# Optimization experiments

Measured on AMD Instinct MI355X. Metric: run time of the kernel, lower is better.

The kernel has to match this reference:

```python
import jax, jax.numpy as jnp
import numpy as np

ALPHA = 0.2        # LeakyReLU slope
N_NODES = 50000
N_REL = 500


def l2norm(x):
    n = jnp.linalg.norm(x, axis=1, keepdims=True)
    return x / jnp.maximum(n, 1e-12)


def gat_layer(x, edge, eemb, a, a2, concat):
    # x: [N, F]; edge: [2, E] (edge[0]=target, edge[1]=source); eemb: [E, R]
    dst = edge[0]
    h = jnp.concatenate([x[dst], x[edge[1]], eemb], axis=1)          # [E, 2F+R]
    m = h @ a.T                                                       # [E, out]
    p = -jax.nn.leaky_relu(m @ a2[0], ALPHA)                          # [E]
    e = jnp.exp(p)
    rowsum = jax.ops.segment_sum(e, dst, num_segments=N_NODES)       # [N]
    rowsum = jnp.where(rowsum == 0.0, 1e-12, rowsum)
    hp = jax.ops.segment_sum(e[:, None] * m, dst, num_segments=N_NODES) / rowsum[:, None]
    return jax.nn.elu(hp) if concat else hp


def setup_inputs() -> dict:
    key = jax.random.key(0)
    ks = jax.random.split(key, 12)
    E, ENH = 150000, 30000
    D, NHID, H = 200, 100, 2
    return {
        "entity_embeddings": jax.random.normal(ks[0], (N_NODES, D), jnp.float32),
        "relation_embeddings": jax.random.normal(ks[1], (N_REL, D), jnp.float32),
        "W_entities": jax.random.normal(ks[2], (D, NHID * H), jnp.float32) * 0.1,
        "W_gat": jax.random.normal(ks[3], (D, NHID * H), jnp.float32) * 0.1,
        "a_heads": jax.random.normal(ks[4], (H, NHID, 2 * D + D), jnp.float32) * 0.1,
        "a2_heads": jax.random.normal(ks[5], (H, 1, NHID), jnp.float32) * 0.1,
        "a_out": jax.random.normal(ks[6], (NHID * H, 3 * NHID * H), jnp.float32) * 0.1,
        "a2_out": jax.random.normal(ks[7], (1, NHID * H), jnp.float32) * 0.1,
        "batch_entities": jax.random.randint(ks[8], (20000,), 0, N_NODES),
        "edge_list": jax.random.randint(ks[9], (2, E), 0, N_NODES),
        "edge_type": jax.random.randint(ks[10], (E,), 0, N_REL),
        "train_indices_nhop": jax.random.randint(ks[11], (ENH, 4), 0, N_REL),
    }


def reference(entity_embeddings, relation_embeddings, W_entities, W_gat,
              a_heads, a2_heads, a_out, a2_out,
              batch_entities, edge_list, edge_type, train_indices_nhop):
    x = l2norm(entity_embeddings)
    # n-hop edges: (target, source) = (col 3, col 0); relation pair = (col 1, col 2)
    edge_nhop = jnp.stack([train_indices_nhop[:, 3], train_indices_nhop[:, 0]])
    edge_all = jnp.concatenate([edge_list, edge_nhop], axis=1)       # [2, E+Enh]
    eemb1 = jnp.concatenate([
        relation_embeddings[edge_type],
        relation_embeddings[train_indices_nhop[:, 1]] + relation_embeddings[train_indices_nhop[:, 2]],
    ], axis=0)
    # multi-head sparse attention (concat=True -> elu inside)
    heads = jax.vmap(lambda a, a2: gat_layer(x, edge_all, eemb1, a, a2, True))(a_heads, a2_heads)
    x1 = jnp.transpose(heads, (1, 0, 2)).reshape(x.shape[0], -1)     # [N, H*nhid]
    out_rel = relation_embeddings @ W_gat                             # [R, H*nhid]
    eemb2 = jnp.concatenate([
        out_rel[edge_type],
        out_rel[train_indices_nhop[:, 1]] + out_rel[train_indices_nhop[:, 2]],
    ], axis=0)
    out_ent = jax.nn.elu(gat_layer(x1, edge_all, eemb2, a_out, a2_out, False))
    mask = jnp.zeros((x.shape[0],), x.dtype).at[batch_entities].set(1.0)
    out_ent = l2norm(x @ W_entities + mask[:, None] * out_ent)
    return out_ent, out_rel, mask
```

## Files before the change

### kernel.cpp

```cpp
#include <hip/hip_runtime.h>
#include <hip/hip_bf16.h>
#include <math.h>

#define DD   200
#define NHID 100
#define OD   200
#define KP   224
#define PBS  448
#define LDSW 40

typedef __attribute__((ext_vector_type(8))) short short8;
typedef __attribute__((ext_vector_type(4))) float f32x4;

static inline int cdiv(int a, int b) { return (a + b - 1) / b; }

__device__ inline float toF(float x) { return x; }
__device__ inline float toF(__hip_bfloat16 x) { return __bfloat162float(x); }
__device__ inline void storeC(float v, float* p) { *p = v; }
__device__ inline void storeC(float v, __hip_bfloat16* p) { *p = __float2bfloat16(v); }
__device__ inline short bf16s(float f) {
    __hip_bfloat16 h = __float2bfloat16(f);
    short s; __builtin_memcpy(&s, &h, 2); return s;
}
__device__ inline float bfLo(unsigned u) { return __uint_as_float(u << 16); }
__device__ inline float bfHi(unsigned u) { return __uint_as_float(u & 0xFFFF0000u); }
__device__ inline float readlaneF(float v, int l) {
    return __uint_as_float((unsigned)__builtin_amdgcn_readlane((int)__float_as_uint(v), l));
}

__global__ __launch_bounds__(256)
void rownorm_inv_k(const float* __restrict__ in, float* __restrict__ sc, int M, int Dd)
{
    int wave = (blockIdx.x * blockDim.x + threadIdx.x) >> 6;
    int lane = threadIdx.x & 63;
    if (wave >= M) return;
    float ss = 0.f;
    for (int k = lane; k < Dd; k += 64) {
        float x = in[(size_t)wave * Dd + k];
        ss += x * x;
    }
    for (int o = 32; o > 0; o >>= 1) ss += __shfl_down(ss, o);
    if (lane == 0) sc[wave] = 1.f / fmaxf(sqrtf(ss), 1e-12f);
}

__global__ void prep_bt_l1(const float* __restrict__ ah, __hip_bfloat16* __restrict__ Bt)
{
    int c = blockIdx.x, k = threadIdx.x;
    if (k >= KP) return;
    int seg = c / 100, idx = c - seg * 100;
    int h = seg & 1, off = (seg >> 1) * 200;
    float v = (k < 200) ? ah[(size_t)(h * 100 + idx) * 600 + off + k] : 0.f;
    Bt[(size_t)c * KP + k] = __float2bfloat16(v);
}
__global__ void prep_bt_l2(const float* __restrict__ ao, __hip_bfloat16* __restrict__ Bt)
{
    int c = blockIdx.x, k = threadIdx.x;
    if (k >= KP) return;
    int row = (c < 200) ? c : c - 200;
    int off = (c < 200) ? 0 : 200;
    float v = (k < 200) ? ao[(size_t)row * 600 + off + k] : 0.f;
    Bt[(size_t)c * KP + k] = __float2bfloat16(v);
}
__global__ void prep_bt_fin(const float* __restrict__ W, __hip_bfloat16* __restrict__ Bt)
{
    int c = blockIdx.x, k = threadIdx.x;
    if (k >= KP) return;
    float v = (c < 200 && k < 200) ? W[(size_t)k * 200 + c] : 0.f;
    Bt[(size_t)c * KP + k] = __float2bfloat16(v);
}

__global__ __launch_bounds__(512)
void l1_both_k(const float* __restrict__ ent, const float* __restrict__ nscale,
               const __hip_bfloat16* __restrict__ Bt,
               const float* __restrict__ a2h,
               __hip_bfloat16* __restrict__ x1,
               __hip_bfloat16* __restrict__ pB,
               float* __restrict__ s1,
               int M)
{
    __shared__ __align__(16) __hip_bfloat16 Bs[400 * LDSW];
    int tid = threadIdx.x, wave = tid >> 6, lane = tid & 63;
    int quad = lane >> 4, l16 = lane & 15;
    int m0 = blockIdx.x * 128;
    int arow = m0 + wave * 16 + l16;
    bool rok = arow < M;
    float nsc = rok ? nscale[arow] : 0.f;
    const float* arp = ent + (size_t)arow * DD;
    int orow = m0 + wave * 16 + quad * 4;

    if (blockIdx.y == 0) {
        f32x4 acc[25];
#pragma unroll
        for (int t = 0; t < 25; t++) acc[t] = (f32x4){0.f, 0.f, 0.f, 0.f};

        short8 stg[4];
#pragma unroll
        for (int i = 0; i < 4; i++) {
            int idx = tid + i * 512;
            if (idx < 1600) {
                int r = idx >> 2, c8 = idx & 3;
                stg[i] = *(const short8*)(Bt + (size_t)r * KP + c8 * 8);
            }
        }
        for (int ch = 0; ch < 7; ch++) {
            int kb = ch * 32 + quad * 8;
            float av[8];
            if (rok && kb + 8 <= DD) {
                const float4* p = (const float4*)(arp + kb);
                float4 u0 = p[0], u1 = p[1];
                av[0] = u0.x; av[1] = u0.y; av[2] = u0.z; av[3] = u0.w;
                av[4] = u1.x; av[5] = u1.y; av[6] = u1.z; av[7] = u1.w;
            } else {
#pragma unroll
                for (int j = 0; j < 8; j++) av[j] = (rok && kb + j < DD) ? arp[kb + j] : 0.f;
            }
#pragma unroll
            for (int i = 0; i < 4; i++) {
                int idx = tid + i * 512;
                if (idx < 1600) {
                    int r = idx >> 2, c8 = idx & 3;
                    *(short8*)(Bs + r * LDSW + c8 * 8) = stg[i];
                }
            }
            __syncthreads();
            if (ch < 6) {
                int kb2 = (ch + 1) * 32;
#pragma unroll
                for (int i = 0; i < 4; i++) {
                    int idx = tid + i * 512;
                    if (idx < 1600) {
                        int r = idx >> 2, c8 = idx & 3;
                        stg[i] = *(const short8*)(Bt + (size_t)r * KP + kb2 + c8 * 8);
                    }
                }
            }
            short8 a;
#pragma unroll
            for (int j = 0; j < 8; j++) a[j] = bf16s(av[j] * nsc);
            const __hip_bfloat16* bp = Bs + (size_t)l16 * LDSW + quad * 8;
#pragma unroll
            for (int t = 0; t < 25; t++) {
                short8 b = *(const short8*)(bp + (size_t)t * 16 * LDSW);
                acc[t] = __builtin_amdgcn_mfma_f32_16x16x32_bf16(a, b, acc[t], 0, 0, 0);
            }
            __syncthreads();
        }

        float d0[4] = {0,0,0,0}, d1[4] = {0,0,0,0}, d2[4] = {0,0,0,0}, d3[4] = {0,0,0,0};
#pragma unroll
        for (int t = 0; t < 25; t++) {
            int c = t * 16 + l16;
            int seg = c / 100, idx = c - seg * 100;
            float w = a2h[(seg & 1) * 100 + idx];
#pragma unroll
            for (int i = 0; i < 4; i++) {
                float v = acc[t][i];
                float vw = v * w;
                if (seg == 0) d0[i] += vw;
                else if (seg == 1) d1[i] += vw;
                else if (seg == 2) d2[i] += vw;
                else d3[i] += vw;
                int gm = orow + i;
                if (gm < M) {
                    if (seg < 2) x1[(size_t)gm * KP + c] = __float2bfloat16(v);
                    else pB[(size_t)gm * PBS + idx * 2 + (seg - 2)] = __float2bfloat16(v);
                }
            }
        }
        if (l16 < 12)
#pragma unroll
            for (int i = 0; i < 4; i++) {
                int gm = orow + i;
                if (gm < M) *(unsigned*)(x1 + (size_t)gm * KP + 200 + 2 * l16) = 0u;
            }
#pragma unroll
        for (int msk = 1; msk < 16; msk <<= 1)
#pragma unroll
            for (int i = 0; i < 4; i++) {
                d0[i] += __shfl_xor(d0[i], msk);
                d1[i] += __shfl_xor(d1[i], msk);
                d2[i] += __shfl_xor(d2[i], msk);
                d3[i] += __shfl_xor(d3[i], msk);
            }
        if (l16 == 0)
#pragma unroll
            for (int i = 0; i < 4; i++) {
                int gm = orow + i;
                if (gm < M) {
                    s1[gm] = d0[i]; s1[M + gm] = d1[i];
                    float2 sv; sv.x = d2[i]; sv.y = d3[i];
                    *(float2*)((char*)pB + (size_t)gm * (PBS * 2) + 400) = sv;
                }
            }
    } else {
        f32x4 acc2[13];
#pragma unroll
        for (int t = 0; t < 13; t++) acc2[t] = (f32x4){0.f, 0.f, 0.f, 0.f};

        short8 stg2[2];
#pragma unroll
        for (int i = 0; i < 2; i++) {
            int idx = tid + i * 512;
            if (idx < 832) {
                int r = idx >> 2, c8 = idx & 3;
                stg2[i] = *(const short8*)(Bt + (size_t)(400 + r) * KP + c8 * 8);
            }
        }
        for (int ch = 0; ch < 7; ch++) {
            int kb = ch * 32 + quad * 8;
            float av[8];
            if (rok && kb + 8 <= DD) {
                const float4* p = (const float4*)(arp + kb);
                float4 u0 = p[0], u1 = p[1];
                av[0] = u0.x; av[1] = u0.y; av[2] = u0.z; av[3] = u0.w;
                av[4] = u1.x; av[5] = u1.y; av[6] = u1.z; av[7] = u1.w;
            } else {
#pragma unroll
                for (int j = 0; j < 8; j++) av[j] = (rok && kb + j < DD) ? arp[kb + j] : 0.f;
            }
#pragma unroll
            for (int i = 0; i < 2; i++) {
                int idx = tid + i * 512;
                if (idx < 832) {
                    int r = idx >> 2, c8 = idx & 3;
                    *(short8*)(Bs + r * LDSW + c8 * 8) = stg2[i];
                }
            }
            __syncthreads();
            if (ch < 6) {
                int kb2 = (ch + 1) * 32;
#pragma unroll
                for (int i = 0; i < 2; i++) {
                    int idx = tid + i * 512;
                    if (idx < 832) {
                        int r = idx >> 2, c8 = idx & 3;
                        stg2[i] = *(const short8*)(Bt + (size_t)(400 + r) * KP + kb2 + c8 * 8);
                    }
                }
            }
            short8 a;
#pragma unroll
            for (int j = 0; j < 8; j++) a[j] = bf16s(av[j] * nsc);
            const __hip_bfloat16* bp = Bs + (size_t)l16 * LDSW + quad * 8;
#pragma unroll
            for (int t = 0; t < 13; t++) {
                short8 b = *(const short8*)(bp + (size_t)t * 16 * LDSW);
                acc2[t] = __builtin_amdgcn_mfma_f32_16x16x32_bf16(a, b, acc2[t], 0, 0, 0);
            }
            __syncthreads();
        }
#pragma unroll
        for (int t = 0; t < 13; t++) {
            int c2 = t * 16 + l16;
#pragma unroll
            for (int i = 0; i < 4; i++) {
                int gm = orow + i;
                if (c2 < OD && gm < M)
                    pB[(size_t)gm * PBS + 224 + c2] = __float2bfloat16(acc2[t][i]);
            }
        }
    }
}

__global__ __launch_bounds__(512)
void l2_proj_k(const __hip_bfloat16* __restrict__ x1,
               const __hip_bfloat16* __restrict__ Bt,
               const float* __restrict__ a2o,
               float* __restrict__ x1A1,
               __hip_bfloat16* __restrict__ x1A2,
               float* __restrict__ s1, int M)
{
    __shared__ __align__(16) __hip_bfloat16 Bs[400 * LDSW];
    int tid = threadIdx.x, wave = tid >> 6, lane = tid & 63;
    int quad = lane >> 4, l16 = lane & 15;
    int m0 = blockIdx.x * 128;
    int arow = m0 + wave * 16 + l16;
    bool rok = arow < M;
    const __hip_bfloat16* arp = x1 + (size_t)arow * KP;

    f32x4 acc[25];
#pragma unroll
    for (int t = 0; t < 25; t++) acc[t] = (f32x4){0.f, 0.f, 0.f, 0.f};

    short8 stg[4];
#pragma unroll
    for (int i = 0; i < 4; i++) {
        int idx = tid + i * 512;
        if (idx < 1600) {
            int r = idx >> 2, c8 = idx & 3;
            stg[i] = *(const short8*)(Bt + (size_t)r * KP + c8 * 8);
        }
    }

    for (int ch = 0; ch < 7; ch++) {
        short8 a = (short8){0,0,0,0,0,0,0,0};
        if (rok) a = *(const short8*)(arp + ch * 32 + quad * 8);
#pragma unroll
        for (int i = 0; i < 4; i++) {
            int idx = tid + i * 512;
            if (idx < 1600) {
                int r = idx >> 2, c8 = idx & 3;
                *(short8*)(Bs + r * LDSW + c8 * 8) = stg[i];
            }
        }
        __syncthreads();
        if (ch < 6) {
            int kb2 = (ch + 1) * 32;
#pragma unroll
            for (int i = 0; i < 4; i++) {
                int idx = tid + i * 512;
                if (idx < 1600) {
                    int r = idx >> 2, c8 = idx & 3;
                    stg[i] = *(const short8*)(Bt + (size_t)r * KP + kb2 + c8 * 8);
                }
            }
        }
        const __hip_bfloat16* bp = Bs + (size_t)l16 * LDSW + quad * 8;
#pragma unroll
        for (int t = 0; t < 25; t++) {
            short8 b = *(const short8*)(bp + (size_t)t * 16 * LDSW);
            acc[t] = __builtin_amdgcn_mfma_f32_16x16x32_bf16(a, b, acc[t], 0, 0, 0);
        }
        __syncthreads();
    }

    int orow = m0 + wave * 16 + quad * 4;
    float dA[4] = {0,0,0,0}, dB[4] = {0,0,0,0};
#pragma unroll
    for (int t = 0; t < 25; t++) {
        int c = t * 16 + l16;
        bool first = c < 200;
        int cc = first ? c : c - 200;
        float w = a2o[cc];
#pragma unroll
        for (int i = 0; i < 4; i++) {
            float v = acc[t][i];
            int gm = orow + i;
            if (first) {
                dA[i] += v * w;
                if (gm < M) x1A1[(size_t)gm * OD + c] = v;
            } else {
                dB[i] += v * w;
                if (gm < M) x1A2[(size_t)gm * PBS + cc] = __float2bfloat16(v);
            }
        }
    }
#pragma unroll
    for (int msk = 1; msk < 16; msk <<= 1)
#pragma unroll
        for (int i = 0; i < 4; i++) {
            dA[i] += __shfl_xor(dA[i], msk);
            dB[i] += __shfl_xor(dB[i], msk);
        }
    if (l16 == 0)
#pragma unroll
        for (int i = 0; i < 4; i++) {
            int gm = orow + i;
            if (gm < M) {
                s1[gm] = dA[i];
                *(float*)((char*)x1A2 + (size_t)gm * (PBS * 2) + 400) = dB[i];
            }
        }
}

#define KPAD 48
template<bool BTr, typename AT, typename CT>
__global__ __launch_bounds__(256)
void gemm_mfma_k(const AT* __restrict__ A, int lda, const float* __restrict__ ascale,
                 const float* __restrict__ B, int ldb, int colOff,
                 CT* __restrict__ C, int ldc, int cs, int co,
                 int M, int Nc, int K)
{
    __shared__ __align__(16) __hip_bfloat16 As[64][KPAD];
    __shared__ __align__(16) __hip_bfloat16 Bs[64][KPAD];
    int tid  = threadIdx.x;
    int wave = tid >> 6, lane = tid & 63;
    int quad = lane >> 4, l16 = lane & 15;
    int n0 = blockIdx.x * 64, m0 = blockIdx.y * 64;
    f32x4 acc[4];
#pragma unroll
    for (int t = 0; t < 4; t++) acc[t] = (f32x4){0.f, 0.f, 0.f, 0.f};

    for (int k0 = 0; k0 < K; k0 += 32) {
        {
            int m = tid >> 2, kc = (tid & 3) * 8;
            int gm = m0 + m;
            float scale = (ascale && gm < M) ? ascale[gm] : 1.f;
#pragma unroll
            for (int j = 0; j < 8; j++) {
                int gk = k0 + kc + j;
                float v = 0.f;
                if (gm < M && gk < K) v = toF(A[(size_t)gm * lda + gk]) * scale;
                As[m][kc + j] = __float2bfloat16(v);
            }
        }
        if (BTr) {
            int n = tid >> 2, kc = (tid & 3) * 8;
            int gn = n0 + n;
#pragma unroll
            for (int j = 0; j < 8; j++) {
                int gk = k0 + kc + j;
                float v = 0.f;
                if (gn < Nc && gk < K) v = B[(size_t)gn * ldb + colOff + gk];
                Bs[n][kc + j] = __float2bfloat16(v);
            }
        } else {
            int n = tid & 63, kq = tid >> 6;
            int gn = n0 + n;
#pragma unroll
            for (int j = 0; j < 8; j++) {
                int gk = k0 + kq * 8 + j;
                float v = 0.f;
                if (gn < Nc && gk < K) v = B[(size_t)gk * ldb + gn];
                Bs[n][kq * 8 + j] = __float2bfloat16(v);
            }
        }
        __syncthreads();
        short8 a = *(const short8*)&As[wave * 16 + l16][quad * 8];
#pragma unroll
        for (int t = 0; t < 4; t++) {
            short8 b = *(const short8*)&Bs[t * 16 + l16][quad * 8];
            acc[t] = __builtin_amdgcn_mfma_f32_16x16x32_bf16(a, b, acc[t], 0, 0, 0);
        }
        __syncthreads();
    }
#pragma unroll
    for (int t = 0; t < 4; t++) {
        int gn = n0 + t * 16 + l16;
        if (gn >= Nc) continue;
#pragma unroll
        for (int i = 0; i < 4; i++) {
            int gm = m0 + wave * 16 + quad * 4 + i;
            if (gm < M) storeC(acc[t][i], &C[(size_t)gm * ldc + (size_t)gn * cs + co]);
        }
    }
}

template<typename T>
__global__ __launch_bounds__(256)
void rowdot_k(const T* __restrict__ mat, int ld, int coff, int ks,
              const float* __restrict__ vec,
              float* __restrict__ outp, int os, int oo, int M, int Dd)
{
    int wave = (blockIdx.x * blockDim.x + threadIdx.x) >> 6;
    int lane = threadIdx.x & 63;
    if (wave >= M) return;
    float s = 0.f;
    for (int k = lane; k < Dd; k += 64)
        s += toF(mat[(size_t)wave * ld + coff + (size_t)k * ks]) * vec[k];
    for (int o = 32; o > 0; o >>= 1) s += __shfl_down(s, o);
    if (lane == 0) outp[wave * os + oo] = s;
}

__device__ inline void decode_edge(const int* __restrict__ el, int E,
                                   const int* __restrict__ etype,
                                   const int* __restrict__ tin, int e,
                                   int& dst, int& src, int& r1, int& r2)
{
    if (e < E) { dst = el[e]; src = el[E + e]; r1 = etype[e]; r2 = -1; }
    else {
        int j = e - E;
        dst = tin[j * 4 + 3]; src = tin[j * 4 + 0];
        r1 = tin[j * 4 + 1];  r2 = tin[j * 4 + 2];
    }
}

__global__ void hist_k(const int* __restrict__ el, int E, const int* __restrict__ etype,
                       const int* __restrict__ tin, int Etot, int* __restrict__ cnt)
{
    int e = blockIdx.x * blockDim.x + threadIdx.x;
    if (e >= Etot) return;
    int dst, src, r1, r2; decode_edge(el, E, etype, tin, e, dst, src, r1, r2);
    atomicAdd(&cnt[dst], 1);
}

__global__ __launch_bounds__(1024)
void scan1_k(const int* __restrict__ cnt, int* __restrict__ start,
             int* __restrict__ aux, int n)
{
    __shared__ int tmp[1024];
    int i = blockIdx.x * 1024 + threadIdx.x;
    int v = (i < n) ? cnt[i] : 0;
    tmp[threadIdx.x] = v;
    __syncthreads();
    for (int o = 1; o < 1024; o <<= 1) {
        int t = (threadIdx.x >= (unsigned)o) ? tmp[threadIdx.x - o] : 0;
        __syncthreads();
        tmp[threadIdx.x] += t;
        __syncthreads();
    }
    if (i < n) start[i] = tmp[threadIdx.x] - v;
    if (threadIdx.x == 1023) aux[blockIdx.x] = tmp[1023];
}

__global__ void scan2_k(int* __restrict__ aux, int nb)
{
    if (threadIdx.x == 0 && blockIdx.x == 0) {
        int s = 0;
        for (int i = 0; i < nb; i++) { int v = aux[i]; aux[i] = s; s += v; }
    }
}

__global__ __launch_bounds__(1024)
void scan3_k(int* __restrict__ start, const int* __restrict__ aux, int n, int Etot)
{
    int i = blockIdx.x * 1024 + threadIdx.x;
    if (i < n) start[i] += aux[blockIdx.x];
    if (i == 0) start[n] = Etot;
}

__global__ void fill_k(const int* __restrict__ el, int E, const int* __restrict__ etype,
                       const int* __restrict__ tin, int Etot,
                       const int* __restrict__ start, int* __restrict__ fill,
                       int2* __restrict__ csr)
{
    int e = blockIdx.x * blockDim.x + threadIdx.x;
    if (e >= Etot) return;
    int dst, src, r1, r2; decode_edge(el, E, etype, tin, e, dst, src, r1, r2);
    int p = start[dst] + atomicAdd(&fill[dst], 1);
    unsigned r2s = (r2 >= 0) ? (unsigned)r2 : 0xFFFFu;
    csr[p] = make_int2(src, (int)((r2s << 16) | (unsigned)r1));
}

__global__ __launch_bounds__(256)
void gather_l1_k(const int* __restrict__ start, const int2* __restrict__ csr,
                 const float* __restrict__ s1,
                 const float* __restrict__ srel2,
                 const __hip_bfloat16* __restrict__ pB,
                 const float* __restrict__ rpf2,
                 __hip_bfloat16* __restrict__ x1, int N)
{
    int n = (blockIdx.x * blockDim.x + threadIdx.x) >> 6;
    int lane = threadIdx.x & 63;
    if (n >= N) return;
    int b0 = __builtin_amdgcn_readfirstlane(start[n]);
    int b1 = __builtin_amdgcn_readfirstlane(start[n + 1]);
    float s1h0 = s1[n], s1h1 = s1[N + n];
    float rsl0 = 0.f, rsl1 = 0.f;
    float2 acc0 = {0.f, 0.f};
    float2 acc1 = {0.f, 0.f};
    int k0 = lane;
    bool k1ok = lane < 36;
    int k1c = k1ok ? (lane + 64) : 0;

    for (int c0 = b0; c0 < b1; c0 += 64) {
        int cnt = min(64, b1 - c0);
        float w0 = 0.f, w1 = 0.f;
        int srcL = 0, eyL = 0;
        if (lane < cnt) {
            int2 eg = csr[c0 + lane];
            srcL = eg.x; eyL = eg.y;
            int r1 = eyL & 0xFFFF;
            unsigned r2u = (unsigned)eyL >> 16;
            float2 sA = *(const float2*)((const char*)pB + (size_t)(unsigned)srcL * (PBS * 2) + 400);
            float2 sr = *(const float2*)(srel2 + r1 * 2);
            float z0 = s1h0 + sA.x + sr.x;
            float z1 = s1h1 + sA.y + sr.y;
            if (r2u != 0xFFFFu) {
                float2 sr2v = *(const float2*)(srel2 + r2u * 2);
                z0 += sr2v.x; z1 += sr2v.y;
            }
            w0 = expf(-(z0 > 0.f ? z0 : 0.2f * z0));
            w1 = expf(-(z1 > 0.f ? z1 : 0.2f * z1));
            rsl0 += w0; rsl1 += w1;
        }
        for (int e0 = 0; e0 < cnt; e0 += 4) {
            int ec = min(4, cnt - e0);
            unsigned pw0[4], pw1[4];
#pragma unroll
            for (int u = 0; u < 4; u++) {
                if (u < ec) {
                    int s = __builtin_amdgcn_readlane(srcL, e0 + u);
                    const __hip_bfloat16* rA = pB + (size_t)(unsigned)s * PBS;
                    pw0[u] = *(const unsigned*)(rA + 2 * k0);
                    pw1[u] = *(const unsigned*)(rA + 2 * k1c);
                }
            }
#pragma unroll
            for (int u = 0; u < 4; u++) {
                if (u < ec) {
                    int ey = __builtin_amdgcn_readlane(eyL, e0 + u);
                    int r1 = ey & 0xFFFF;
                    unsigned r2u = (unsigned)ey >> 16;
                    float we0 = readlaneF(w0, e0 + u);
                    float we1 = readlaneF(w1, e0 + u);
                    const float2* q1 = (const float2*)(rpf2 + (unsigned)r1 * 200);
                    float2 q1a = q1[k0], q1b = q1[k1c];
                    float v00 = bfLo(pw0[u]) + q1a.x;
                    float v01 = bfHi(pw0[u]) + q1a.y;
                    float v10 = bfLo(pw1[u]) + q1b.x;
                    float v11 = bfHi(pw1[u]) + q1b.y;
                    if (r2u != 0xFFFFu) {
                        const float2* q2 = (const float2*)(rpf2 + r2u * 200);
                        float2 q2a = q2[k0], q2b = q2[k1c];
                        v00 += q2a.x; v01 += q2a.y;
                        v10 += q2b.x; v11 += q2b.y;
                    }
                    acc0.x += we0 * v00; acc0.y += we1 * v01;
                    acc1.x += we0 * v10; acc1.y += we1 * v11;
                }
            }
        }
    }

#pragma unroll
    for (int o = 1; o < 64; o <<= 1) {
        rsl0 += __shfl_xor(rsl0, o);
        rsl1 += __shfl_xor(rsl1, o);
    }
    float i0 = rsl0 > 0.f ? 1.f / rsl0 : 0.f;
    float i1 = rsl1 > 0.f ? 1.f / rsl1 : 0.f;
    __hip_bfloat16* xr = x1 + (size_t)n * KP;
    float hp;
    hp = rsl0 > 0.f ? toF(xr[k0]) + acc0.x * i0 : 0.f;
    xr[k0] = __float2bfloat16(hp > 0.f ? hp : expf(hp) - 1.f);
    hp = rsl1 > 0.f ? toF(xr[100 + k0]) + acc0.y * i1 : 0.f;
    xr[100 + k0] = __float2bfloat16(hp > 0.f ? hp : expf(hp) - 1.f);
    if (k1ok) {
        int k1 = lane + 64;
        hp = rsl0 > 0.f ? toF(xr[k1]) + acc1.x * i0 : 0.f;
        xr[k1] = __float2bfloat16(hp > 0.f ? hp : expf(hp) - 1.f);
        hp = rsl1 > 0.f ? toF(xr[100 + k1]) + acc1.y * i1 : 0.f;
        xr[100 + k1] = __float2bfloat16(hp > 0.f ? hp : expf(hp) - 1.f);
    }
}

__global__ __launch_bounds__(256)
void gather_l2_k(const int* __restrict__ start, const int2* __restrict__ csr,
                 const float* __restrict__ s1,
                 const float* __restrict__ srel,
                 const __hip_bfloat16* __restrict__ x1A2,
                 const float* __restrict__ rpf,
                 const float* __restrict__ maskf,
                 float* __restrict__ outent, int N)
{
    int n = (blockIdx.x * blockDim.x + threadIdx.x) >> 6;
    int lane = threadIdx.x & 63;
    if (n >= N) return;
    int b0 = __builtin_amdgcn_readfirstlane(start[n]);
    int b1 = __builtin_amdgcn_readfirstlane(start[n + 1]);
    float s1n = s1[n];
    float rsl = 0.f;
    float2 a0 = {0.f, 0.f};
    float2 a1 = {0.f, 0.f};
    int j0 = 2 * lane;
    bool j1ok = lane < 36;
    int j1 = j1ok ? (128 + 2 * lane) : 0;

    for (int c0 = b0; c0 < b1; c0 += 64) {
        int cnt = min(64, b1 - c0);
        float w = 0.f;
        int srcL = 0, eyL = 0;
        if (lane < cnt) {
            int2 eg = csr[c0 + lane];
            srcL = eg.x; eyL = eg.y;
            int r1 = eyL & 0xFFFF;
            unsigned r2u = (unsigned)eyL >> 16;
            float s2v = *(const float*)((const char*)x1A2 + (size_t)(unsigned)srcL * (PBS * 2) + 400);
            float sr = srel[r1];
            if (r2u != 0xFFFFu) sr += srel[r2u];
            float z = s1n + s2v + sr;
            w = expf(-(z > 0.f ? z : 0.2f * z));
            rsl += w;
        }
        for (int e0 = 0; e0 < cnt; e0 += 4) {
            int ec = min(4, cnt - e0);
            unsigned xw0[4], xw1[4];
#pragma unroll
            for (int u = 0; u < 4; u++) {
                if (u < ec) {
                    int s = __builtin_amdgcn_readlane(srcL, e0 + u);
                    const __hip_bfloat16* xs = x1A2 + (size_t)(unsigned)s * PBS;
                    xw0[u] = *(const unsigned*)(xs + j0);
                    xw1[u] = *(const unsigned*)(xs + j1);
                }
            }
#pragma unroll
            for (int u = 0; u < 4; u++) {
                if (u < ec) {
                    int ey = __builtin_amdgcn_readlane(eyL, e0 + u);
                    int r1 = ey & 0xFFFF;
                    unsigned r2u = (unsigned)ey >> 16;
                    float we = readlaneF(w, e0 + u);
                    const float* q1 = rpf + (unsigned)r1 * 200;
                    float2 q1a = *(const float2*)(q1 + j0);
                    float2 q1b = *(const float2*)(q1 + j1);
                    float v0x = bfLo(xw0[u]) + q1a.x;
                    float v0y = bfHi(xw0[u]) + q1a.y;
                    float v1x = bfLo(xw1[u]) + q1b.x;
                    float v1y = bfHi(xw1[u]) + q1b.y;
                    if (r2u != 0xFFFFu) {
                        const float* q2 = rpf + r2u * 200;
                        float2 q2a = *(const float2*)(q2 + j0);
                        float2 q2b = *(const float2*)(q2 + j1);
                        v0x += q2a.x; v0y += q2a.y;
                        v1x += q2b.x; v1y += q2b.y;
                    }
                    a0.x += we * v0x; a0.y += we * v0y;
                    a1.x += we * v1x; a1.y += we * v1y;
                }
            }
        }
    }

#pragma unroll
    for (int o = 1; o < 64; o <<= 1) rsl += __shfl_xor(rsl, o);
    float inv = rsl > 0.f ? 1.f / rsl : 0.f;
    float mk = maskf[n];
    float* orow = outent + (size_t)n * 200;
    const __hip_bfloat16* ew = x1A2 + (size_t)n * PBS + 224;

    float2 o0 = *(const float2*)(orow + j0);
    unsigned e0b = *(const unsigned*)(ew + j0);
    float h0x = rsl > 0.f ? o0.x + a0.x * inv : 0.f;
    float h0y = rsl > 0.f ? o0.y + a0.y * inv : 0.f;
    float v0x = mk * (h0x > 0.f ? h0x : expf(h0x) - 1.f) + bfLo(e0b);
    float v0y = mk * (h0y > 0.f ? h0y : expf(h0y) - 1.f) + bfHi(e0b);
    float ssq = v0x * v0x + v0y * v0y;
    float v1x = 0.f, v1y = 0.f;
    if (j1ok) {
        float2 o1 = *(const float2*)(orow + j1);
        unsigned e1b = *(const unsigned*)(ew + j1);
        float h1x = rsl > 0.f ? o1.x + a1.x * inv : 0.f;
        float h1y = rsl > 0.f ? o1.y + a1.y * inv : 0.f;
        v1x = mk * (h1x > 0.f ? h1x : expf(h1x) - 1.f) + bfLo(e1b);
        v1y = mk * (h1y > 0.f ? h1y : expf(h1y) - 1.f) + bfHi(e1b);
        ssq += v1x * v1x + v1y * v1y;
    }
#pragma unroll
    for (int o = 1; o < 64; o <<= 1) ssq += __shfl_xor(ssq, o);
    float sc = 1.f / fmaxf(sqrtf(ssq), 1e-12f);
    float2 r0; r0.x = v0x * sc; r0.y = v0y * sc;
    *(float2*)(orow + j0) = r0;
    if (j1ok) {
        float2 r1; r1.x = v1x * sc; r1.y = v1y * sc;
        *(float2*)(orow + j1) = r1;
    }
}

__global__ void scatter_mask_k(const int* __restrict__ batch, int NB,
                               float* __restrict__ masko)
{
    int i = blockIdx.x * blockDim.x + threadIdx.x;
    if (i >= NB) return;
    masko[batch[i]] = 1.0f;
}

extern "C" void kernel_launch(void* const* d_in, const int* in_sizes, int n_in,
                              void* d_out, int out_size, void* d_ws, size_t ws_size,
                              hipStream_t stream)
{
    const float* ent      = (const float*)d_in[0];
    const float* rel      = (const float*)d_in[1];
    const float* W_ent    = (const float*)d_in[2];
    const float* W_gat    = (const float*)d_in[3];
    const float* a_heads  = (const float*)d_in[4];
    const float* a2_heads = (const float*)d_in[5];
    const float* a_out    = (const float*)d_in[6];
    const float* a2_out   = (const float*)d_in[7];
    const int* batch = (const int*)d_in[8];
    const int* el    = (const int*)d_in[9];
    const int* etype = (const int*)d_in[10];
    const int* tin   = (const int*)d_in[11];

    const int N   = in_sizes[0] / DD;
    const int R   = in_sizes[1] / DD;
    const int NB  = in_sizes[8];
    const int E   = in_sizes[9] / 2;
    const int ENH = in_sizes[11] / 4;
    const int Etot = E + ENH;

    char* ws = (char*)d_ws;
    size_t off = 0;
    auto take = [&](size_t bytes) { size_t o = off; off += (bytes + 255) & ~(size_t)255; return o; };
    size_t o_R1   = take((size_t)N * KP * 2);
    size_t o_R2   = take((size_t)N * PBS * 2);
    size_t o_rpf  = take((size_t)2 * R * 100 * 4);
    size_t o_bt1  = take((size_t)400 * KP * 2);
    size_t o_btf  = take((size_t)208 * KP * 2);
    size_t o_bt2  = take((size_t)400 * KP * 2);
    size_t o_nsc  = take((size_t)N * 4);
    size_t o_s1   = take((size_t)2 * N * 4);
    size_t o_srel = take((size_t)2 * R * 4);
    size_t o_csr  = take((size_t)Etot * 8);
    size_t o_str  = take((size_t)(N + 1) * 4);
    size_t o_aux  = take((size_t)64 * 4);

    __hip_bfloat16* x1   = (__hip_bfloat16*)(ws + o_R1);
    __hip_bfloat16* pB   = (__hip_bfloat16*)(ws + o_R2);
    __hip_bfloat16* x1A2 = (__hip_bfloat16*)(ws + o_R2);
    float* rpf2   = (float*)(ws + o_rpf);
    __hip_bfloat16* bt1 = (__hip_bfloat16*)(ws + o_bt1);
    __hip_bfloat16* btf = (__hip_bfloat16*)(ws + o_btf);
    __hip_bfloat16* bt2 = (__hip_bfloat16*)(ws + o_bt2);
    float* nscale = (float*)(ws + o_nsc);
    float* s1     = (float*)(ws + o_s1);
    float* srel2  = (float*)(ws + o_srel);
    int2*  csr    = (int2*)(ws + o_csr);
    int*   cnt    = (int*)(ws + o_s1);
    int*   startA = (int*)(ws + o_str);
    int*   aux    = (int*)(ws + o_aux);

    float* out       = (float*)d_out;
    float* out_ent   = out;
    float* out_rel_o = out + (size_t)N * OD;
    float* out_mask  = out + (size_t)N * OD + (size_t)R * OD;

    const int nblk2 = cdiv(N, 128);
    const int nbScan = cdiv(N, 1024);

    rownorm_inv_k<<<cdiv(N, 4), 256, 0, stream>>>(ent, nscale, N, DD);
    prep_bt_l1<<<400, 256, 0, stream>>>(a_heads, bt1);
    prep_bt_fin<<<208, 256, 0, stream>>>(W_ent, btf);
    prep_bt_l2<<<400, 256, 0, stream>>>(a_out, bt2);
    gemm_mfma_k<false, float, float><<<dim3(cdiv(OD, 64), cdiv(R, 64)), 256, 0, stream>>>(
        rel, DD, nullptr, W_gat, OD, 0, out_rel_o, OD, 1, 0, R, OD, DD);

    hipMemsetAsync(cnt, 0, (size_t)N * 4, stream);
    hist_k<<<cdiv(Etot, 256), 256, 0, stream>>>(el, E, etype, tin, Etot, cnt);
    scan1_k<<<nbScan, 1024, 0, stream>>>(cnt, startA, aux, N);
    scan2_k<<<1, 64, 0, stream>>>(aux, nbScan);
    scan3_k<<<nbScan, 1024, 0, stream>>>(startA, aux, N, Etot);
    hipMemsetAsync(cnt, 0, (size_t)N * 4, stream);
    fill_k<<<cdiv(Etot, 256), 256, 0, stream>>>(el, E, etype, tin, Etot, startA, cnt, csr);

    l1_both_k<<<dim3(nblk2, 2), 512, 0, stream>>>(ent, nscale, bt1, a2_heads, x1, pB, s1, N);
    for (int h = 0; h < 2; h++) {
        const float* ah  = a_heads + (size_t)h * NHID * 600;
        const float* a2h = a2_heads + (size_t)h * NHID;
        gemm_mfma_k<true, float, float><<<dim3(cdiv(NHID, 64), cdiv(R, 64)), 256, 0, stream>>>(
            rel, DD, nullptr, ah, 600, 400, rpf2, 200, 2, h, R, NHID, DD);
        rowdot_k<float><<<cdiv(R, 4), 256, 0, stream>>>(
            rpf2, 200, h, 2, a2h, srel2, 2, h, R, NHID);
    }
    gather_l1_k<<<cdiv(N, 4), 256, 0, stream>>>(
        startA, csr, s1, srel2, pB, rpf2, x1, N);

    l2_proj_k<<<nblk2, 512, 0, stream>>>(x1, bt2, a2_out, out_ent, x1A2, s1, N);
    gemm_mfma_k<true, float, float><<<dim3(cdiv(OD, 64), cdiv(R, 64)), 256, 0, stream>>>(
        out_rel_o, OD, nullptr, a_out, 600, 400, rpf2, OD, 1, 0, R, OD, OD);
    rowdot_k<float><<<cdiv(R, 4), 256, 0, stream>>>(rpf2, OD, 0, 1, a2_out, srel2, 1, 0, R, OD);

    hipMemsetAsync(out_mask, 0, (size_t)N * 4, stream);
    scatter_mask_k<<<cdiv(NB, 256), 256, 0, stream>>>(batch, NB, out_mask);
    gather_l2_k<<<cdiv(N, 4), 256, 0, stream>>>(
        startA, csr, s1, srel2, x1A2, rpf2, out_mask, out_ent, N);
}
```

Baseline: 450.7 us.

## Split projection GEMMs into uniform 208-column blocks across more grid slices

The layer-1 and layer-2 projection kernels now split the output columns into equal 208-wide slices selected by blockIdx.y (3 slices for layer 1, 2 for layer 2), replacing the uneven 400+200 split and the single 400-column block. Each block holds 13 accumulator tiles instead of 25 and uses a smaller LDS buffer, which should raise occupancy and balance the work across blocks. The weight-transpose prep kernels are re-laid out with padded 208-row groups to match. The cost is that every slice re-reads the A rows (entity embeddings or x1) and repeats the normalisation and conversion work.

```diff
diff --git a/kernel.cpp b/kernel.cpp
--- a/kernel.cpp
+++ b/kernel.cpp
@@ -47,18 +47,23 @@
 {
     int c = blockIdx.x, k = threadIdx.x;
     if (k >= KP) return;
-    int seg = c / 100, idx = c - seg * 100;
-    int h = seg & 1, off = (seg >> 1) * 200;
-    float v = (k < 200) ? ah[(size_t)(h * 100 + idx) * 600 + off + k] : 0.f;
+    int g = (c >= 208) ? 1 : 0;
+    int cc = c - g * 208;
+    float v = 0.f;
+    if (cc < 200 && k < 200) {
+        int hh = (cc >= 100) ? 1 : 0;
+        int idx = cc - hh * 100;
+        v = ah[(size_t)(hh * 100 + idx) * 600 + g * 200 + k];
+    }
     Bt[(size_t)c * KP + k] = __float2bfloat16(v);
 }
 __global__ void prep_bt_l2(const float* __restrict__ ao, __hip_bfloat16* __restrict__ Bt)
 {
     int c = blockIdx.x, k = threadIdx.x;
     if (k >= KP) return;
-    int row = (c < 200) ? c : c - 200;
-    int off = (c < 200) ? 0 : 200;
-    float v = (k < 200) ? ao[(size_t)row * 600 + off + k] : 0.f;
+    int g = (c >= 208) ? 1 : 0;
+    int cc = c - g * 208;
+    float v = (cc < 200 && k < 200) ? ao[(size_t)cc * 600 + g * 200 + k] : 0.f;
     Bt[(size_t)c * KP + k] = __float2bfloat16(v);
 }
 __global__ void prep_bt_fin(const float* __restrict__ W, __hip_bfloat16* __restrict__ Bt)
@@ -78,188 +83,139 @@
                float* __restrict__ s1,
                int M)
 {
-    __shared__ __align__(16) __hip_bfloat16 Bs[400 * LDSW];
+    __shared__ __align__(16) __hip_bfloat16 Bs[208 * LDSW];
     int tid = threadIdx.x, wave = tid >> 6, lane = tid & 63;
     int quad = lane >> 4, l16 = lane & 15;
+    int f = blockIdx.y;
+    int rowbase = f * 208;
     int m0 = blockIdx.x * 128;
     int arow = m0 + wave * 16 + l16;
     bool rok = arow < M;
     float nsc = rok ? nscale[arow] : 0.f;
     const float* arp = ent + (size_t)arow * DD;
     int orow = m0 + wave * 16 + quad * 4;
-
-    if (blockIdx.y == 0) {
-        f32x4 acc[25];
-#pragma unroll
-        for (int t = 0; t < 25; t++) acc[t] = (f32x4){0.f, 0.f, 0.f, 0.f};
-
-        short8 stg[4];
-#pragma unroll
-        for (int i = 0; i < 4; i++) {
-            int idx = tid + i * 512;
-            if (idx < 1600) {
-                int r = idx >> 2, c8 = idx & 3;
-                stg[i] = *(const short8*)(Bt + (size_t)r * KP + c8 * 8);
-            }
-        }
-        for (int ch = 0; ch < 7; ch++) {
-            int kb = ch * 32 + quad * 8;
-            float av[8];
-            if (rok && kb + 8 <= DD) {
-                const float4* p = (const float4*)(arp + kb);
-                float4 u0 = p[0], u1 = p[1];
-                av[0] = u0.x; av[1] = u0.y; av[2] = u0.z; av[3] = u0.w;
-                av[4] = u1.x; av[5] = u1.y; av[6] = u1.z; av[7] = u1.w;
-            } else {
-#pragma unroll
-                for (int j = 0; j < 8; j++) av[j] = (rok && kb + j < DD) ? arp[kb + j] : 0.f;
-            }
-#pragma unroll
-            for (int i = 0; i < 4; i++) {
-                int idx = tid + i * 512;
-                if (idx < 1600) {
-                    int r = idx >> 2, c8 = idx & 3;
-                    *(short8*)(Bs + r * LDSW + c8 * 8) = stg[i];
-                }
-            }
-            __syncthreads();
-            if (ch < 6) {
-                int kb2 = (ch + 1) * 32;
-#pragma unroll
-                for (int i = 0; i < 4; i++) {
-                    int idx = tid + i * 512;
-                    if (idx < 1600) {
-                        int r = idx >> 2, c8 = idx & 3;
-                        stg[i] = *(const short8*)(Bt + (size_t)r * KP + kb2 + c8 * 8);
-                    }
-                }
-            }
-            short8 a;
-#pragma unroll
-            for (int j = 0; j < 8; j++) a[j] = bf16s(av[j] * nsc);
-            const __hip_bfloat16* bp = Bs + (size_t)l16 * LDSW + quad * 8;
-#pragma unroll
-            for (int t = 0; t < 25; t++) {
-                short8 b = *(const short8*)(bp + (size_t)t * 16 * LDSW);
-                acc[t] = __builtin_amdgcn_mfma_f32_16x16x32_bf16(a, b, acc[t], 0, 0, 0);
-            }
-            __syncthreads();
-        }
-
-        float d0[4] = {0,0,0,0}, d1[4] = {0,0,0,0}, d2[4] = {0,0,0,0}, d3[4] = {0,0,0,0};
-#pragma unroll
-        for (int t = 0; t < 25; t++) {
-            int c = t * 16 + l16;
-            int seg = c / 100, idx = c - seg * 100;
-            float w = a2h[(seg & 1) * 100 + idx];
-#pragma unroll
-            for (int i = 0; i < 4; i++) {
-                float v = acc[t][i];
-                float vw = v * w;
-                if (seg == 0) d0[i] += vw;
-                else if (seg == 1) d1[i] += vw;
-                else if (seg == 2) d2[i] += vw;
-                else d3[i] += vw;
-                int gm = orow + i;
-                if (gm < M) {
-                    if (seg < 2) x1[(size_t)gm * KP + c] = __float2bfloat16(v);
-                    else pB[(size_t)gm * PBS + idx * 2 + (seg - 2)] = __float2bfloat16(v);
-                }
-            }
-        }
-        if (l16 < 12)
-#pragma unroll
-            for (int i = 0; i < 4; i++) {
-                int gm = orow + i;
-                if (gm < M) *(unsigned*)(x1 + (size_t)gm * KP + 200 + 2 * l16) = 0u;
-            }
-#pragma unroll
-        for (int msk = 1; msk < 16; msk <<= 1)
-#pragma unroll
-            for (int i = 0; i < 4; i++) {
-                d0[i] += __shfl_xor(d0[i], msk);
-                d1[i] += __shfl_xor(d1[i], msk);
-                d2[i] += __shfl_xor(d2[i], msk);
-                d3[i] += __shfl_xor(d3[i], msk);
-            }
-        if (l16 == 0)
-#pragma unroll
-            for (int i = 0; i < 4; i++) {
-                int gm = orow + i;
-                if (gm < M) {
-                    s1[gm] = d0[i]; s1[M + gm] = d1[i];
-                    float2 sv; sv.x = d2[i]; sv.y = d3[i];
-                    *(float2*)((char*)pB + (size_t)gm * (PBS * 2) + 400) = sv;
-                }
-            }
-    } else {
-        f32x4 acc2[13];
-#pragma unroll
-        for (int t = 0; t < 13; t++) acc2[t] = (f32x4){0.f, 0.f, 0.f, 0.f};
-
-        short8 stg2[2];
+    const __hip_bfloat16* Bsrc = Bt + (size_t)rowbase * KP;
+
+    f32x4 acc[13];
+#pragma unroll
+    for (int t = 0; t < 13; t++) acc[t] = (f32x4){0.f, 0.f, 0.f, 0.f};
+
+    short8 stg[2];
+#pragma unroll
+    for (int i = 0; i < 2; i++) {
+        int idx = tid + i * 512;
+        if (idx < 832) {
+            int r = idx >> 2, c8 = idx & 3;
+            stg[i] = *(const short8*)(Bsrc + (size_t)r * KP + c8 * 8);
+        }
+    }
+    for (int ch = 0; ch < 7; ch++) {
+        int kb = ch * 32 + quad * 8;
+        float av[8];
+        if (rok && kb + 8 <= DD) {
+            const float4* p = (const float4*)(arp + kb);
+            float4 u0 = p[0], u1 = p[1];
+            av[0] = u0.x; av[1] = u0.y; av[2] = u0.z; av[3] = u0.w;
+            av[4] = u1.x; av[5] = u1.y; av[6] = u1.z; av[7] = u1.w;
+        } else {
+#pragma unroll
+            for (int j = 0; j < 8; j++) av[j] = (rok && kb + j < DD) ? arp[kb + j] : 0.f;
+        }
 #pragma unroll
         for (int i = 0; i < 2; i++) {
             int idx = tid + i * 512;
             if (idx < 832) {
                 int r = idx >> 2, c8 = idx & 3;
-                stg2[i] = *(const short8*)(Bt + (size_t)(400 + r) * KP + c8 * 8);
-            }
-        }
-        for (int ch = 0; ch < 7; ch++) {
-            int kb = ch * 32 + quad * 8;
-            float av[8];
-            if (rok && kb + 8 <= DD) {
-                const float4* p = (const float4*)(arp + kb);
-                float4 u0 = p[0], u1 = p[1];
-                av[0] = u0.x; av[1] = u0.y; av[2] = u0.z; av[3] = u0.w;
-                av[4] = u1.x; av[5] = u1.y; av[6] = u1.z; av[7] = u1.w;
-            } else {
-#pragma unroll
-                for (int j = 0; j < 8; j++) av[j] = (rok && kb + j < DD) ? arp[kb + j] : 0.f;
-            }
+                *(short8*)(Bs + r * LDSW + c8 * 8) = stg[i];
+            }
+        }
+        __syncthreads();
+        if (ch < 6) {
+            int kb2 = (ch + 1) * 32;
 #pragma unroll
             for (int i = 0; i < 2; i++) {
                 int idx = tid + i * 512;
                 if (idx < 832) {
                     int r = idx >> 2, c8 = idx & 3;
-                    *(short8*)(Bs + r * LDSW + c8 * 8) = stg2[i];
+                    stg[i] = *(const short8*)(Bsrc + (size_t)r * KP + kb2 + c8 * 8);
                 }
             }
-            __syncthreads();
-            if (ch < 6) {
-                int kb2 = (ch + 1) * 32;
-#pragma unroll
-                for (int i = 0; i < 2; i++) {
-                    int idx = tid + i * 512;
-                    if (idx < 832) {
-                        int r = idx >> 2, c8 = idx & 3;
-                        stg2[i] = *(const short8*)(Bt + (size_t)(400 + r) * KP + kb2 + c8 * 8);
-                    }
-                }
-            }
-            short8 a;
-#pragma unroll
-            for (int j = 0; j < 8; j++) a[j] = bf16s(av[j] * nsc);
-            const __hip_bfloat16* bp = Bs + (size_t)l16 * LDSW + quad * 8;
-#pragma unroll
-            for (int t = 0; t < 13; t++) {
-                short8 b = *(const short8*)(bp + (size_t)t * 16 * LDSW);
-                acc2[t] = __builtin_amdgcn_mfma_f32_16x16x32_bf16(a, b, acc2[t], 0, 0, 0);
-            }
-            __syncthreads();
-        }
+        }
+        short8 a;
+#pragma unroll
+        for (int j = 0; j < 8; j++) a[j] = bf16s(av[j] * nsc);
+        const __hip_bfloat16* bp = Bs + (size_t)l16 * LDSW + quad * 8;
 #pragma unroll
         for (int t = 0; t < 13; t++) {
-            int c2 = t * 16 + l16;
+            short8 b = *(const short8*)(bp + (size_t)t * 16 * LDSW);
+            acc[t] = __builtin_amdgcn_mfma_f32_16x16x32_bf16(a, b, acc[t], 0, 0, 0);
+        }
+        __syncthreads();
+    }
+
+    if (f == 2) {
+#pragma unroll
+        for (int t = 0; t < 13; t++) {
+            int cc = t * 16 + l16;
 #pragma unroll
             for (int i = 0; i < 4; i++) {
                 int gm = orow + i;
-                if (c2 < OD && gm < M)
-                    pB[(size_t)gm * PBS + 224 + c2] = __float2bfloat16(acc2[t][i]);
-            }
-        }
-    }
+                if (cc < OD && gm < M)
+                    pB[(size_t)gm * PBS + 224 + cc] = __float2bfloat16(acc[t][i]);
+            }
+        }
+        return;
+    }
+
+    float dLo[4] = {0,0,0,0}, dHi[4] = {0,0,0,0};
+#pragma unroll
+    for (int t = 0; t < 13; t++) {
+        int cc = t * 16 + l16;
+        bool cok = cc < 200;
+        float w = cok ? a2h[cc] : 0.f;
+#pragma unroll
+        for (int i = 0; i < 4; i++) {
+            float v = acc[t][i];
+            float vw = v * w;
+            if (cc < 100) dLo[i] += vw;
+            else if (cok) dHi[i] += vw;
+            int gm = orow + i;
+            if (cok && gm < M) {
+                if (f == 0) x1[(size_t)gm * KP + cc] = __float2bfloat16(v);
+                else {
+                    int hh = (cc >= 100) ? 1 : 0;
+                    pB[(size_t)gm * PBS + (cc - hh * 100) * 2 + hh] = __float2bfloat16(v);
+                }
+            }
+        }
+    }
+    if (f == 0) {
+        if (l16 < 12)
+#pragma unroll
+            for (int i = 0; i < 4; i++) {
+                int gm = orow + i;
+                if (gm < M) *(unsigned*)(x1 + (size_t)gm * KP + 200 + 2 * l16) = 0u;
+            }
+    }
+#pragma unroll
+    for (int msk = 1; msk < 16; msk <<= 1)
+#pragma unroll
+        for (int i = 0; i < 4; i++) {
+            dLo[i] += __shfl_xor(dLo[i], msk);
+            dHi[i] += __shfl_xor(dHi[i], msk);
+        }
+    if (l16 == 0)
+#pragma unroll
+        for (int i = 0; i < 4; i++) {
+            int gm = orow + i;
+            if (gm < M) {
+                if (f == 0) { s1[gm] = dLo[i]; s1[M + gm] = dHi[i]; }
+                else {
+                    float2 sv; sv.x = dLo[i]; sv.y = dHi[i];
+                    *(float2*)((char*)pB + (size_t)gm * (PBS * 2) + 400) = sv;
+                }
+            }
+        }
 }
 
 __global__ __launch_bounds__(512)
@@ -270,35 +226,37 @@
                __hip_bfloat16* __restrict__ x1A2,
                float* __restrict__ s1, int M)
 {
-    __shared__ __align__(16) __hip_bfloat16 Bs[400 * LDSW];
+    __shared__ __align__(16) __hip_bfloat16 Bs[208 * LDSW];
     int tid = threadIdx.x, wave = tid >> 6, lane = tid & 63;
     int quad = lane >> 4, l16 = lane & 15;
+    int f = blockIdx.y;
+    int rowbase = f * 208;
     int m0 = blockIdx.x * 128;
     int arow = m0 + wave * 16 + l16;
     bool rok = arow < M;
     const __hip_bfloat16* arp = x1 + (size_t)arow * KP;
-
-    f32x4 acc[25];
-#pragma unroll
-    for (int t = 0; t < 25; t++) acc[t] = (f32x4){0.f, 0.f, 0.f, 0.f};
-
-    short8 stg[4];
-#pragma unroll
-    for (int i = 0; i < 4; i++) {
+    const __hip_bfloat16* Bsrc = Bt + (size_t)rowbase * KP;
+
+    f32x4 acc[13];
+#pragma unroll
+    for (int t = 0; t < 13; t++) acc[t] = (f32x4){0.f, 0.f, 0.f, 0.f};
+
+    short8 stg[2];
+#pragma unroll
+    for (int i = 0; i < 2; i++) {
         int idx = tid + i * 512;
-        if (idx < 1600) {
+        if (idx < 832) {
             int r = idx >> 2, c8 = idx & 3;
-            stg[i] = *(const short8*)(Bt + (size_t)r * KP + c8 * 8);
-        }
-    }
-
+            stg[i] = *(const short8*)(Bsrc + (size_t)r * KP + c8 * 8);
+        }
+    }
     for (int ch = 0; ch < 7; ch++) {
         short8 a = (short8){0,0,0,0,0,0,0,0};
         if (rok) a = *(const short8*)(arp + ch * 32 + quad * 8);
 #pragma unroll
-        for (int i = 0; i < 4; i++) {
+        for (int i = 0; i < 2; i++) {
             int idx = tid + i * 512;
-            if (idx < 1600) {
+            if (idx < 832) {
                 int r = idx >> 2, c8 = idx & 3;
                 *(short8*)(Bs + r * LDSW + c8 * 8) = stg[i];
             }
@@ -307,17 +265,17 @@
         if (ch < 6) {
             int kb2 = (ch + 1) * 32;
 #pragma unroll
-            for (int i = 0; i < 4; i++) {
+            for (int i = 0; i < 2; i++) {
                 int idx = tid + i * 512;
-                if (idx < 1600) {
+                if (idx < 832) {
                     int r = idx >> 2, c8 = idx & 3;
-                    stg[i] = *(const short8*)(Bt + (size_t)r * KP + kb2 + c8 * 8);
+                    stg[i] = *(const short8*)(Bsrc + (size_t)r * KP + kb2 + c8 * 8);
                 }
             }
         }
         const __hip_bfloat16* bp = Bs + (size_t)l16 * LDSW + quad * 8;
 #pragma unroll
-        for (int t = 0; t < 25; t++) {
+        for (int t = 0; t < 13; t++) {
             short8 b = *(const short8*)(bp + (size_t)t * 16 * LDSW);
             acc[t] = __builtin_amdgcn_mfma_f32_16x16x32_bf16(a, b, acc[t], 0, 0, 0);
         }
@@ -325,40 +283,34 @@
     }
 
     int orow = m0 + wave * 16 + quad * 4;
-    float dA[4] = {0,0,0,0}, dB[4] = {0,0,0,0};
-#pragma unroll
-    for (int t = 0; t < 25; t++) {
-        int c = t * 16 + l16;
-        bool first = c < 200;
-        int cc = first ? c : c - 200;
-        float w = a2o[cc];
+    float d[4] = {0,0,0,0};
+#pragma unroll
+    for (int t = 0; t < 13; t++) {
+        int cc = t * 16 + l16;
+        bool cok = cc < 200;
+        float w = cok ? a2o[cc] : 0.f;
 #pragma unroll
         for (int i = 0; i < 4; i++) {
             float v = acc[t][i];
+            d[i] += v * w;
             int gm = orow + i;
-            if (first) {
-                dA[i] += v * w;
-                if (gm < M) x1A1[(size_t)gm * OD + c] = v;
-            } else {
-                dB[i] += v * w;
-                if (gm < M) x1A2[(size_t)gm * PBS + cc] = __float2bfloat16(v);
+            if (cok && gm < M) {
+                if (f == 0) x1A1[(size_t)gm * OD + cc] = v;
+                else x1A2[(size_t)gm * PBS + cc] = __float2bfloat16(v);
             }
         }
     }
 #pragma unroll
     for (int msk = 1; msk < 16; msk <<= 1)
 #pragma unroll
-        for (int i = 0; i < 4; i++) {
-            dA[i] += __shfl_xor(dA[i], msk);
-            dB[i] += __shfl_xor(dB[i], msk);
-        }
+        for (int i = 0; i < 4; i++) d[i] += __shfl_xor(d[i], msk);
     if (l16 == 0)
 #pragma unroll
         for (int i = 0; i < 4; i++) {
             int gm = orow + i;
             if (gm < M) {
-                s1[gm] = dA[i];
-                *(float*)((char*)x1A2 + (size_t)gm * (PBS * 2) + 400) = dB[i];
+                if (f == 0) s1[gm] = d[i];
+                else *(float*)((char*)x1A2 + (size_t)gm * (PBS * 2) + 400) = d[i];
             }
         }
 }
@@ -776,9 +728,9 @@
     size_t o_R1   = take((size_t)N * KP * 2);
     size_t o_R2   = take((size_t)N * PBS * 2);
     size_t o_rpf  = take((size_t)2 * R * 100 * 4);
-    size_t o_bt1  = take((size_t)400 * KP * 2);
+    size_t o_bt1  = take((size_t)416 * KP * 2);
     size_t o_btf  = take((size_t)208 * KP * 2);
-    size_t o_bt2  = take((size_t)400 * KP * 2);
+    size_t o_bt2  = take((size_t)416 * KP * 2);
     size_t o_nsc  = take((size_t)N * 4);
     size_t o_s1   = take((size_t)2 * N * 4);
     size_t o_srel = take((size_t)2 * R * 4);
@@ -810,9 +762,9 @@
     const int nbScan = cdiv(N, 1024);
 
     rownorm_inv_k<<<cdiv(N, 4), 256, 0, stream>>>(ent, nscale, N, DD);
-    prep_bt_l1<<<400, 256, 0, stream>>>(a_heads, bt1);
+    prep_bt_l1<<<416, 256, 0, stream>>>(a_heads, bt1);
     prep_bt_fin<<<208, 256, 0, stream>>>(W_ent, btf);
-    prep_bt_l2<<<400, 256, 0, stream>>>(a_out, bt2);
+    prep_bt_l2<<<416, 256, 0, stream>>>(a_out, bt2);
     gemm_mfma_k<false, float, float><<<dim3(cdiv(OD, 64), cdiv(R, 64)), 256, 0, stream>>>(
         rel, DD, nullptr, W_gat, OD, 0, out_rel_o, OD, 1, 0, R, OD, DD);
 
@@ -824,7 +776,7 @@
     hipMemsetAsync(cnt, 0, (size_t)N * 4, stream);
     fill_k<<<cdiv(Etot, 256), 256, 0, stream>>>(el, E, etype, tin, Etot, startA, cnt, csr);
 
-    l1_both_k<<<dim3(nblk2, 2), 512, 0, stream>>>(ent, nscale, bt1, a2_heads, x1, pB, s1, N);
+    l1_both_k<<<dim3(nblk2, 3), 512, 0, stream>>>(ent, nscale, bt1, a2_heads, x1, pB, s1, N);
     for (int h = 0; h < 2; h++) {
         const float* ah  = a_heads + (size_t)h * NHID * 600;
         const float* a2h = a2_heads + (size_t)h * NHID;
@@ -836,7 +788,7 @@
     gather_l1_k<<<cdiv(N, 4), 256, 0, stream>>>(
         startA, csr, s1, srel2, pB, rpf2, x1, N);
 
-    l2_proj_k<<<nblk2, 512, 0, stream>>>(x1, bt2, a2_out, out_ent, x1A2, s1, N);
+    l2_proj_k<<<dim3(nblk2, 2), 512, 0, stream>>>(x1, bt2, a2_out, out_ent, x1A2, s1, N);
     gemm_mfma_k<true, float, float><<<dim3(cdiv(OD, 64), cdiv(R, 64)), 256, 0, stream>>>(
         out_rel_o, OD, nullptr, a_out, 600, 400, rpf2, OD, 1, 0, R, OD, OD);
     rowdot_k<float><<<cdiv(R, 4), 256, 0, stream>>>(rpf2, OD, 0, 1, a2_out, srel2, 1, 0, R, OD);
```

Measured after the change: 444.7 us. About the same (-1.3%).
